# Optimization experiments

Measured on AMD Instinct MI355X. Metric: run time of the kernel, lower is better.

The kernel has to match this reference:

```python
import jax, jax.numpy as jnp
import numpy as np

TAU = 2.0          # LIF membrane time constant (spikingjelly default)
V_TH = 1.0         # v_threshold
V_RESET = 0.0      # hard reset value
ATAN_ALPHA = 2.0   # surrogate.ATan default alpha
EPS = 1e-12        # F.normalize eps

@jax.custom_vjp
def spike_fn(x):
    # Heaviside forward, ATan surrogate backward
    return (x >= 0).astype(x.dtype)

def _spike_fwd(x):
    return spike_fn(x), x

def _spike_bwd(x, g):
    sg = (ATAN_ALPHA / 2.0) / (1.0 + (jnp.pi / 2.0 * ATAN_ALPHA * x) ** 2)
    return (g * sg,)

spike_fn.defvjp(_spike_fwd, _spike_bwd)

def setup_inputs() -> dict:
    key = jax.random.key(0)
    k1, k2 = jax.random.split(key)
    T, B, F, H = 32, 512, 2048, 2048
    x_seq = jax.random.normal(k1, (T, B, F), dtype=jnp.float32)
    lim = float(np.sqrt(6.0 / (F + H)))  # xavier_uniform
    W = jax.random.uniform(k2, (H, F), dtype=jnp.float32, minval=-lim, maxval=lim)
    b = jnp.zeros((H,), dtype=jnp.float32)
    return {"x_seq": x_seq, "W": W, "b": b}

def reference(x_seq, W, b):
    # Linear: [T,B,F] @ [F,H] -> [T,B,H]
    cur = jnp.einsum('tbf,hf->tbh', x_seq, W) + b
    # F.normalize(dim=-1): L2 normalize the injected current per neuron vector
    norm = jnp.maximum(jnp.sqrt(jnp.sum(cur * cur, axis=-1, keepdims=True)), EPS)
    cur = cur / norm

    def step(v, c):
        # LIF charge: v <- v + (x - (v - v_reset)) / tau
        v = v + (c - (v - V_RESET)) / TAU
        s = spike_fn(v - V_TH)
        sd = jax.lax.stop_gradient(s)  # detach_reset=True
        v = v * (1.0 - sd) + V_RESET * sd  # hard reset
        return v, s

    v0 = jnp.zeros(cur.shape[1:], dtype=cur.dtype)  # [B,H]
    _, spk_seq = jax.lax.scan(step, v0, cur)  # spk_seq: [T,B,H]
    count = spk_seq.sum(axis=0)  # [B,H]
    return spk_seq, count
```

## Files before the change

### kernel.cpp

```cpp
#include <hip/hip_runtime.h>
#include <hip/hip_bf16.h>

#define T_SZ 32
#define B_SZ 512
#define F_SZ 2048
#define H_SZ 2048
#define M_SZ (T_SZ * B_SZ)

#define BM 256
#define BN 128
#define BK 64
#define NT (F_SZ / BK)
#define ABYTES (BM * BK)
#define BBYTES (BN * BK)
#define TILE_BYTES (ABYTES + BBYTES)

typedef int   i32x8  __attribute__((ext_vector_type(8)));
typedef float f32x16 __attribute__((ext_vector_type(16)));

__device__ __forceinline__ void gload_lds16(const void* g, void* l) {
    __builtin_amdgcn_global_load_lds(
        (const __attribute__((address_space(1))) unsigned int*)g,
        (__attribute__((address_space(3))) unsigned int*)l,
        16, 0, 0);
}

__device__ __forceinline__ float bf16_bits_to_f32(unsigned short u) {
    return __uint_as_float(((unsigned)u) << 16);
}

__device__ __forceinline__ void sbar() {
    __builtin_amdgcn_sched_barrier(0);
    __builtin_amdgcn_s_barrier();
    __builtin_amdgcn_sched_barrier(0);
}

#define MFMA_FP8(a, b, c) __builtin_amdgcn_mfma_scale_f32_32x32x64_f8f6f4( \
        (a), (b), (c), 0 , 0 , 0, 0x7f7f7f7f, 0, 0x7f7f7f7f)

#define NBLK_X ((M_SZ * F_SZ / 8) / 256)
#define NBLK_W ((H_SZ * F_SZ / 8) / 256)
#define NBLK_S ((M_SZ / 4) / 256)

__device__ __forceinline__ void cvt8(const float* __restrict__ in,
                                     unsigned int* __restrict__ out,
                                     float scale, int i) {
    float4 v0 = ((const float4*)in)[2 * i];
    float4 v1 = ((const float4*)in)[2 * i + 1];
    int w0 = __builtin_amdgcn_cvt_pk_fp8_f32(v0.x * scale, v0.y * scale, 0, false);
    w0     = __builtin_amdgcn_cvt_pk_fp8_f32(v0.z * scale, v0.w * scale, w0, true);
    int w1 = __builtin_amdgcn_cvt_pk_fp8_f32(v1.x * scale, v1.y * scale, 0, false);
    w1     = __builtin_amdgcn_cvt_pk_fp8_f32(v1.z * scale, v1.w * scale, w1, true);
    ((uint2*)out)[i] = make_uint2((unsigned)w0, (unsigned)w1);
}

__global__ __launch_bounds__(256) void prep_kernel(const float* __restrict__ x,
                                                   const float* __restrict__ W,
                                                   unsigned int* __restrict__ x8,
                                                   unsigned int* __restrict__ W8,
                                                   float4* __restrict__ ss4) {
    const int bid = blockIdx.x;
    if (bid < NBLK_X) {
        cvt8(x, x8, 1.0f, bid * 256 + threadIdx.x);
    } else if (bid < NBLK_X + NBLK_W) {
        cvt8(W, W8, 256.0f, (bid - NBLK_X) * 256 + threadIdx.x);
    } else {
        ss4[(bid - NBLK_X - NBLK_W) * 256 + threadIdx.x] = make_float4(0.f, 0.f, 0.f, 0.f);
    }
}

__global__ __launch_bounds__(256, 2) void gemm_fp8_kernel(const unsigned char* __restrict__ A,
                                                          const unsigned char* __restrict__ Bt,
                                                          const float* __restrict__ bias,
                                                          __hip_bfloat16* __restrict__ C,
                                                          float* __restrict__ ss)
{
    __shared__ __align__(16) unsigned char smem[3 * TILE_BYTES];

    const int tid  = threadIdx.x;
    const int lane = tid & 63;
    const int wave = tid >> 6;
    const int wm   = wave >> 1;
    const int wn   = wave & 1;
    const int l31  = lane & 31;
    const int kh   = lane >> 5;

    const int flat = blockIdx.y * 16 + blockIdx.x;
    const int swz  = (flat & 7) * 128 + (flat >> 3);
    const int n0   = (swz & 15) * BN;
    const int m0   = (swz >> 4) * BM;

    const unsigned char* const Ap = A  + (size_t)m0 * F_SZ;
    const unsigned char* const Bp = Bt + (size_t)n0 * F_SZ;

    int sAg[4], sAl[4];
    #pragma unroll
    for (int j = 0; j < 4; ++j) {
        const int c = j * 256 + tid;
        const int row = c >> 2;
        const int u = (c & 3) ^ ((row >> 1) & 3);
        sAg[j] = row * F_SZ + u * 16;
        sAl[j] = c * 16;
    }
    int sBg[2], sBl[2];
    #pragma unroll
    for (int j = 0; j < 2; ++j) {
        const int c = j * 256 + tid;
        const int row = c >> 2;
        const int u = (c & 3) ^ ((row >> 1) & 3);
        sBg[j] = row * F_SZ + u * 16;
        sBl[j] = c * 16;
    }

    int aoff[4][2], boff[2][2];
    #pragma unroll
    for (int mi = 0; mi < 4; ++mi) {
        const int ra = wm * 128 + mi * 32 + l31;
        #pragma unroll
        for (int j = 0; j < 2; ++j)
            aoff[mi][j] = ra * BK + (((kh * 2 + j) ^ ((ra >> 1) & 3)) * 16);
    }
    #pragma unroll
    for (int ni = 0; ni < 2; ++ni) {
        const int rb = wn * 64 + ni * 32 + l31;
        #pragma unroll
        for (int j = 0; j < 2; ++j)
            boff[ni][j] = rb * BK + (((kh * 2 + j) ^ ((rb >> 1) & 3)) * 16);
    }

    auto stageA = [&](int p, int kt) {
        unsigned char* const d = smem + p * TILE_BYTES;
        #pragma unroll
        for (int j = 0; j < 4; ++j) gload_lds16(Ap + kt * BK + sAg[j], d + sAl[j]);
    };
    auto stageB = [&](int p, int kt) {
        unsigned char* const d = smem + p * TILE_BYTES + ABYTES;
        #pragma unroll
        for (int j = 0; j < 2; ++j) gload_lds16(Bp + kt * BK + sBg[j], d + sBl[j]);
    };

    f32x16 acc[4][2] = {};

    stageA(0, 0); stageB(0, 0);
    stageA(1, 1); stageB(1, 1);
    asm volatile("s_waitcnt vmcnt(6)" ::: "memory");
    sbar();

    int cur = 0;
    #pragma unroll 1
    for (int kt = 0; kt < NT; ++kt) {
        unsigned char* const buf = smem + cur * TILE_BYTES;
        unsigned char* const Bs  = buf + ABYTES;

        i32x8 a01[2], a23[2], bq[2];
        #pragma unroll
        for (int ni = 0; ni < 2; ++ni) {
            ((int4*)&bq[ni])[0] = *(const int4*)(Bs + boff[ni][0]);
            ((int4*)&bq[ni])[1] = *(const int4*)(Bs + boff[ni][1]);
        }
        #pragma unroll
        for (int mi = 0; mi < 2; ++mi) {
            ((int4*)&a01[mi])[0] = *(const int4*)(buf + aoff[mi][0]);
            ((int4*)&a01[mi])[1] = *(const int4*)(buf + aoff[mi][1]);
            ((int4*)&a23[mi])[0] = *(const int4*)(buf + aoff[2 + mi][0]);
            ((int4*)&a23[mi])[1] = *(const int4*)(buf + aoff[2 + mi][1]);
        }

        if (kt + 2 < NT) {
            const int p2 = (cur + 2 >= 3) ? cur - 1 : cur + 2;
            stageA(p2, kt + 2);
            stageB(p2, kt + 2);
        }

        __builtin_amdgcn_s_setprio(1);
        acc[0][0] = MFMA_FP8(a01[0], bq[0], acc[0][0]);
        acc[0][1] = MFMA_FP8(a01[0], bq[1], acc[0][1]);
        acc[1][0] = MFMA_FP8(a01[1], bq[0], acc[1][0]);
        acc[1][1] = MFMA_FP8(a01[1], bq[1], acc[1][1]);
        acc[2][0] = MFMA_FP8(a23[0], bq[0], acc[2][0]);
        acc[2][1] = MFMA_FP8(a23[0], bq[1], acc[2][1]);
        acc[3][0] = MFMA_FP8(a23[1], bq[0], acc[3][0]);
        acc[3][1] = MFMA_FP8(a23[1], bq[1], acc[3][1]);
        __builtin_amdgcn_s_setprio(0);

        if (kt < NT - 2)       { asm volatile("s_waitcnt vmcnt(6)" ::: "memory"); }
        else if (kt == NT - 2) { asm volatile("s_waitcnt vmcnt(0)" ::: "memory"); }
        if (kt < NT - 1) sbar();

        cur = (cur + 1 >= 3) ? 0 : cur + 1;
    }

    float bv[2];
    #pragma unroll
    for (int ni = 0; ni < 2; ++ni) bv[ni] = bias[n0 + wn * 64 + ni * 32 + l31];
    #pragma unroll
    for (int mi = 0; mi < 4; ++mi) {
        const int gmb = m0 + wm * 128 + mi * 32 + 4 * kh;
        #pragma unroll
        for (int r = 0; r < 16; ++r) {
            const int grow = gmb + (r & 3) + 8 * (r >> 2);
            float p = 0.f;
            #pragma unroll
            for (int ni = 0; ni < 2; ++ni) {
                const int gn = n0 + wn * 64 + ni * 32 + l31;
                const float val = acc[mi][ni][r] * (1.0f / 256.0f) + bv[ni];
                C[(size_t)grow * H_SZ + gn] = __float2bfloat16(val);
                p += val * val;
            }
            p += __shfl_xor(p, 1, 64);
            p += __shfl_xor(p, 2, 64);
            p += __shfl_xor(p, 4, 64);
            p += __shfl_xor(p, 8, 64);
            p += __shfl_xor(p, 16, 64);
            if (l31 == 0) atomicAdd(ss + grow, p);
        }
    }
}

__global__ __launch_bounds__(256) void lif_scan_kernel(const __hip_bfloat16* __restrict__ cur,
                                                       const float* __restrict__ ss,
                                                       float* __restrict__ spk,
                                                       float* __restrict__ cnt)
{
    __shared__ float s_inv[T_SZ];
    const int gid = blockIdx.x * 256 + threadIdx.x;
    const int b   = gid >> 9;
    const int h0  = (gid & 511) * 4;

    if (threadIdx.x < T_SZ)
        s_inv[threadIdx.x] = 1.0f / fmaxf(sqrtf(ss[threadIdx.x * B_SZ + b]), 1e-12f);
    __syncthreads();

    const size_t stride = (size_t)B_SZ * H_SZ;
    const size_t base   = (size_t)b * H_SZ + h0;
    const __hip_bfloat16* p = cur + base;

    ushort4 pk[3];
    pk[0] = *(const ushort4*)(p);
    pk[1] = *(const ushort4*)(p + stride);
    pk[2] = *(const ushort4*)(p + 2 * stride);

    float v[4]  = {0, 0, 0, 0};
    float cn[4] = {0, 0, 0, 0};
    #pragma unroll
    for (int t = 0; t < T_SZ; ++t) {
        const ushort4 k = pk[t % 3];
        if (t + 3 < T_SZ) pk[t % 3] = *(const ushort4*)(p + (size_t)(t + 3) * stride);
        const float inv = s_inv[t];
        float so[4];
        {
            float c;
            c = bf16_bits_to_f32(k.x) * inv; v[0] += (c - v[0]) * 0.5f;
            c = bf16_bits_to_f32(k.y) * inv; v[1] += (c - v[1]) * 0.5f;
            c = bf16_bits_to_f32(k.z) * inv; v[2] += (c - v[2]) * 0.5f;
            c = bf16_bits_to_f32(k.w) * inv; v[3] += (c - v[3]) * 0.5f;
        }
        #pragma unroll
        for (int j = 0; j < 4; ++j) {
            float s = (v[j] >= 1.0f) ? 1.0f : 0.0f;
            so[j] = s;
            cn[j] += s;
            v[j] = (s != 0.f) ? 0.f : v[j];
        }
        *(float4*)(spk + base + (size_t)t * stride) = make_float4(so[0], so[1], so[2], so[3]);
    }
    *(float4*)(cnt + base) = make_float4(cn[0], cn[1], cn[2], cn[3]);
}

extern "C" void kernel_launch(void* const* d_in, const int* in_sizes, int n_in,
                              void* d_out, int out_size, void* d_ws, size_t ws_size,
                              hipStream_t stream) {
    const float* x    = (const float*)d_in[0];
    const float* W    = (const float*)d_in[1];
    const float* bias = (const float*)d_in[2];

    float* spk = (float*)d_out;
    float* cnt = spk + (size_t)T_SZ * B_SZ * H_SZ;

    char* ws = (char*)d_ws;
    unsigned char* x8    = (unsigned char*)ws;
    unsigned char* W8    = x8 + (size_t)M_SZ * F_SZ;
    __hip_bfloat16* curb = (__hip_bfloat16*)(W8 + (size_t)H_SZ * F_SZ);
    float* ss            = (float*)((char*)curb + (size_t)M_SZ * H_SZ * 2);

    prep_kernel<<<NBLK_X + NBLK_W + NBLK_S, 256, 0, stream>>>(
        x, W, (unsigned int*)x8, (unsigned int*)W8, (float4*)ss);
    gemm_fp8_kernel<<<dim3(H_SZ / BN, M_SZ / BM), 256, 0, stream>>>(x8, W8, bias, curb, ss);
    lif_scan_kernel<<<(B_SZ * H_SZ / 4) / 256, 256, 0, stream>>>(curb, ss, spk, cnt);
}
```

Baseline: 357.3 us.

## Halve GEMM M tile and switch to simple double-buffered pipeline

Shrinks the FP8 GEMM block tile from 256x128 to 128x128 and moves from a three-stage LDS ring with explicit vmcnt waits to a two-buffer scheme synchronised with __syncthreads. The launch bound is raised to allow 3 blocks per CU, and the block swizzle is adjusted for twice as many M tiles. The aim is more resident blocks and less LDS and register use per block. In exchange, each loaded operand is reused less, global traffic per FLOP rises, and the shallower prefetch with full barriers may expose more memory latency.

```diff
diff --git a/kernel.cpp b/kernel.cpp
--- a/kernel.cpp
+++ b/kernel.cpp
@@ -7,7 +7,7 @@
 #define H_SZ 2048
 #define M_SZ (T_SZ * B_SZ)
 
-#define BM 256
+#define BM 128
 #define BN 128
 #define BK 64
 #define NT (F_SZ / BK)
@@ -27,12 +27,6 @@
 
 __device__ __forceinline__ float bf16_bits_to_f32(unsigned short u) {
     return __uint_as_float(((unsigned)u) << 16);
-}
-
-__device__ __forceinline__ void sbar() {
-    __builtin_amdgcn_sched_barrier(0);
-    __builtin_amdgcn_s_barrier();
-    __builtin_amdgcn_sched_barrier(0);
 }
 
 #define MFMA_FP8(a, b, c) __builtin_amdgcn_mfma_scale_f32_32x32x64_f8f6f4( \
@@ -69,13 +63,13 @@
     }
 }
 
-__global__ __launch_bounds__(256, 2) void gemm_fp8_kernel(const unsigned char* __restrict__ A,
+__global__ __launch_bounds__(256, 3) void gemm_fp8_kernel(const unsigned char* __restrict__ A,
                                                           const unsigned char* __restrict__ Bt,
                                                           const float* __restrict__ bias,
                                                           __hip_bfloat16* __restrict__ C,
                                                           float* __restrict__ ss)
 {
-    __shared__ __align__(16) unsigned char smem[3 * TILE_BYTES];
+    __shared__ __align__(16) unsigned char smem[2 * TILE_BYTES];
 
     const int tid  = threadIdx.x;
     const int lane = tid & 63;
@@ -86,36 +80,27 @@
     const int kh   = lane >> 5;
 
     const int flat = blockIdx.y * 16 + blockIdx.x;
-    const int swz  = (flat & 7) * 128 + (flat >> 3);
+    const int swz  = (flat & 7) * 256 + (flat >> 3);
     const int n0   = (swz & 15) * BN;
     const int m0   = (swz >> 4) * BM;
 
     const unsigned char* const Ap = A  + (size_t)m0 * F_SZ;
     const unsigned char* const Bp = Bt + (size_t)n0 * F_SZ;
 
-    int sAg[4], sAl[4];
-    #pragma unroll
-    for (int j = 0; j < 4; ++j) {
-        const int c = j * 256 + tid;
-        const int row = c >> 2;
-        const int u = (c & 3) ^ ((row >> 1) & 3);
-        sAg[j] = row * F_SZ + u * 16;
-        sAl[j] = c * 16;
-    }
-    int sBg[2], sBl[2];
+    int sg[2], sl[2];
     #pragma unroll
     for (int j = 0; j < 2; ++j) {
         const int c = j * 256 + tid;
         const int row = c >> 2;
         const int u = (c & 3) ^ ((row >> 1) & 3);
-        sBg[j] = row * F_SZ + u * 16;
-        sBl[j] = c * 16;
-    }
-
-    int aoff[4][2], boff[2][2];
-    #pragma unroll
-    for (int mi = 0; mi < 4; ++mi) {
-        const int ra = wm * 128 + mi * 32 + l31;
+        sg[j] = row * F_SZ + u * 16;
+        sl[j] = c * 16;
+    }
+
+    int aoff[2][2], boff[2][2];
+    #pragma unroll
+    for (int mi = 0; mi < 2; ++mi) {
+        const int ra = wm * 64 + mi * 32 + l31;
         #pragma unroll
         for (int j = 0; j < 2; ++j)
             aoff[mi][j] = ra * BK + (((kh * 2 + j) ^ ((ra >> 1) & 3)) * 16);
@@ -128,74 +113,52 @@
             boff[ni][j] = rb * BK + (((kh * 2 + j) ^ ((rb >> 1) & 3)) * 16);
     }
 
-    auto stageA = [&](int p, int kt) {
+    auto stage = [&](int p, int kt) {
         unsigned char* const d = smem + p * TILE_BYTES;
         #pragma unroll
-        for (int j = 0; j < 4; ++j) gload_lds16(Ap + kt * BK + sAg[j], d + sAl[j]);
+        for (int j = 0; j < 2; ++j) gload_lds16(Ap + kt * BK + sg[j], d + sl[j]);
+        #pragma unroll
+        for (int j = 0; j < 2; ++j) gload_lds16(Bp + kt * BK + sg[j], d + ABYTES + sl[j]);
     };
-    auto stageB = [&](int p, int kt) {
-        unsigned char* const d = smem + p * TILE_BYTES + ABYTES;
-        #pragma unroll
-        for (int j = 0; j < 2; ++j) gload_lds16(Bp + kt * BK + sBg[j], d + sBl[j]);
-    };
-
-    f32x16 acc[4][2] = {};
-
-    stageA(0, 0); stageB(0, 0);
-    stageA(1, 1); stageB(1, 1);
-    asm volatile("s_waitcnt vmcnt(6)" ::: "memory");
-    sbar();
-
-    int cur = 0;
+
+    f32x16 acc[2][2] = {};
+
+    stage(0, 0);
+
     #pragma unroll 1
     for (int kt = 0; kt < NT; ++kt) {
-        unsigned char* const buf = smem + cur * TILE_BYTES;
-        unsigned char* const Bs  = buf + ABYTES;
-
-        i32x8 a01[2], a23[2], bq[2];
+        __syncthreads();
+        const unsigned char* const buf = smem + (kt & 1) * TILE_BYTES;
+        const unsigned char* const Bs  = buf + ABYTES;
+
+        i32x8 af[2], bf[2];
+        #pragma unroll
+        for (int mi = 0; mi < 2; ++mi) {
+            ((int4*)&af[mi])[0] = *(const int4*)(buf + aoff[mi][0]);
+            ((int4*)&af[mi])[1] = *(const int4*)(buf + aoff[mi][1]);
+        }
         #pragma unroll
         for (int ni = 0; ni < 2; ++ni) {
-            ((int4*)&bq[ni])[0] = *(const int4*)(Bs + boff[ni][0]);
-            ((int4*)&bq[ni])[1] = *(const int4*)(Bs + boff[ni][1]);
-        }
-        #pragma unroll
-        for (int mi = 0; mi < 2; ++mi) {
-            ((int4*)&a01[mi])[0] = *(const int4*)(buf + aoff[mi][0]);
-            ((int4*)&a01[mi])[1] = *(const int4*)(buf + aoff[mi][1]);
-            ((int4*)&a23[mi])[0] = *(const int4*)(buf + aoff[2 + mi][0]);
-            ((int4*)&a23[mi])[1] = *(const int4*)(buf + aoff[2 + mi][1]);
-        }
-
-        if (kt + 2 < NT) {
-            const int p2 = (cur + 2 >= 3) ? cur - 1 : cur + 2;
-            stageA(p2, kt + 2);
-            stageB(p2, kt + 2);
-        }
+            ((int4*)&bf[ni])[0] = *(const int4*)(Bs + boff[ni][0]);
+            ((int4*)&bf[ni])[1] = *(const int4*)(Bs + boff[ni][1]);
+        }
+
+        if (kt + 1 < NT) stage((kt + 1) & 1, kt + 1);
 
         __builtin_amdgcn_s_setprio(1);
-        acc[0][0] = MFMA_FP8(a01[0], bq[0], acc[0][0]);
-        acc[0][1] = MFMA_FP8(a01[0], bq[1], acc[0][1]);
-        acc[1][0] = MFMA_FP8(a01[1], bq[0], acc[1][0]);
-        acc[1][1] = MFMA_FP8(a01[1], bq[1], acc[1][1]);
-        acc[2][0] = MFMA_FP8(a23[0], bq[0], acc[2][0]);
-        acc[2][1] = MFMA_FP8(a23[0], bq[1], acc[2][1]);
-        acc[3][0] = MFMA_FP8(a23[1], bq[0], acc[3][0]);
-        acc[3][1] = MFMA_FP8(a23[1], bq[1], acc[3][1]);
+        acc[0][0] = MFMA_FP8(af[0], bf[0], acc[0][0]);
+        acc[0][1] = MFMA_FP8(af[0], bf[1], acc[0][1]);
+        acc[1][0] = MFMA_FP8(af[1], bf[0], acc[1][0]);
+        acc[1][1] = MFMA_FP8(af[1], bf[1], acc[1][1]);
         __builtin_amdgcn_s_setprio(0);
-
-        if (kt < NT - 2)       { asm volatile("s_waitcnt vmcnt(6)" ::: "memory"); }
-        else if (kt == NT - 2) { asm volatile("s_waitcnt vmcnt(0)" ::: "memory"); }
-        if (kt < NT - 1) sbar();
-
-        cur = (cur + 1 >= 3) ? 0 : cur + 1;
     }
 
     float bv[2];
     #pragma unroll
     for (int ni = 0; ni < 2; ++ni) bv[ni] = bias[n0 + wn * 64 + ni * 32 + l31];
     #pragma unroll
-    for (int mi = 0; mi < 4; ++mi) {
-        const int gmb = m0 + wm * 128 + mi * 32 + 4 * kh;
+    for (int mi = 0; mi < 2; ++mi) {
+        const int gmb = m0 + wm * 64 + mi * 32 + 4 * kh;
         #pragma unroll
         for (int r = 0; r < 16; ++r) {
             const int grow = gmb + (r & 3) + 8 * (r >> 2);
```

Result: slower. 369.5 us (+3.4%).
